# Kernel optimization log

Hardware: AMD Instinct MI355X
Metric: run time of the kernel (lower is better)

Reference implementation:

```python
import jax, jax.numpy as jnp
import numpy as np
from jax import lax

B, DIM, F, H, W = 2, 256, 4, 16, 16
HEADS, DIM_HEAD, GROUPS = 8, 64, 4
INNER = HEADS * DIM_HEAD            # 512
OFF_DIMS = INNER // GROUPS          # 128
CPB_DIM = DIM // 4                  # 64
DS = (2, 2, 2)                      # downsample_factor
OFFSET_SCALE = (2.0, 2.0, 2.0)


def norm_coords(coords, sizes):
    # coords: (..., 3) in (f, h, w) index units -> normalized to [-1, 1]
    s = jnp.array([max(sizes[0] - 1, 1), max(sizes[1] - 1, 1), max(sizes[2] - 1, 1)], dtype=coords.dtype)
    return 2.0 * coords / s - 1.0


def grid_sample_3d(vol, grid):
    # Faithful to F.grid_sample(..., mode='bilinear', padding_mode='zeros', align_corners=False)
    # vol: (N, C, D, H, W); grid: (N, P, 3) with last dim (x, y, z) -> (W, H, D) axes
    N, C, D, Hh, Ww = vol.shape
    P = grid.shape[1]
    ix = ((grid[..., 0] + 1.0) * Ww - 1.0) * 0.5
    iy = ((grid[..., 1] + 1.0) * Hh - 1.0) * 0.5
    iz = ((grid[..., 2] + 1.0) * D - 1.0) * 0.5
    x0, y0, z0 = jnp.floor(ix), jnp.floor(iy), jnp.floor(iz)
    tx, ty, tz = ix - x0, iy - y0, iz - z0
    vol_flat = vol.reshape(N, C, D * Hh * Ww)
    out = jnp.zeros((N, C, P), vol.dtype)
    for dz in (0, 1):
        for dy in (0, 1):
            for dx in (0, 1):
                xc, yc, zc = x0 + dx, y0 + dy, z0 + dz
                wgt = (jnp.where(dx, tx, 1.0 - tx) * jnp.where(dy, ty, 1.0 - ty) * jnp.where(dz, tz, 1.0 - tz))
                valid = ((xc >= 0) & (xc < Ww) & (yc >= 0) & (yc < Hh) & (zc >= 0) & (zc < D))
                xi = jnp.clip(xc, 0, Ww - 1).astype(jnp.int32)
                yi = jnp.clip(yc, 0, Hh - 1).astype(jnp.int32)
                zi = jnp.clip(zc, 0, D - 1).astype(jnp.int32)
                idx = (zi * Hh + yi) * Ww + xi                      # (N, P)
                vals = jnp.take_along_axis(vol_flat, jnp.broadcast_to(idx[:, None, :], (N, C, P)), axis=2)
                out = out + vals * (wgt * valid)[:, None, :]
    return out


def setup_inputs():
    key = jax.random.key(0)
    ks = jax.random.split(key, 16)
    r = lambda i, shape: jax.random.normal(ks[i], shape, dtype=jnp.float32) * 0.05
    return {
        'x': jax.random.normal(ks[0], (B, DIM, F, H, W), dtype=jnp.float32),
        'wq': r(1, (GROUPS, OFF_DIMS, DIM // GROUPS)),
        'wk': r(2, (GROUPS, OFF_DIMS, DIM // GROUPS)),
        'wv': r(3, (GROUPS, OFF_DIMS, DIM // GROUPS)),
        'off_dw_w': r(4, (OFF_DIMS, 1, 4, 4, 4)),
        'off_dw_b': r(5, (OFF_DIMS,)),
        'off_pw_w': r(6, (3, OFF_DIMS)),
        'cpb_w0': r(7, (3, CPB_DIM)),
        'cpb_b0': r(8, (CPB_DIM,)),
        'cpb_w1': r(9, (CPB_DIM, CPB_DIM)),
        'cpb_b1': r(10, (CPB_DIM,)),
        'cpb_w2': r(11, (CPB_DIM, HEADS // GROUPS)),
        'cpb_b2': r(12, (HEADS // GROUPS,)),
        'wo': r(13, (DIM, INNER)),
        'bo': r(14, (DIM,)),
    }


def reference(x, wq, wk, wv, off_dw_w, off_dw_b, off_pw_w, cpb_w0, cpb_b0, cpb_w1, cpb_b1, cpb_w2, cpb_b2, wo, bo):
    b = x.shape[0]
    f, h, w = x.shape[-3:]
    Pq = f * h * w
    scale = DIM_HEAD ** -0.5

    # grouped 1x1 conv to queries: channels are (g, d_out) ordered
    xg = x.reshape(b, GROUPS, DIM // GROUPS, Pq)
    q = jnp.einsum('bgip,goi->bgop', xg, wq)                        # (b, G, 128, Pq)

    # learned offsets: depthwise strided conv -> GELU -> 1x1 -> tanh -> scale
    gq = q.reshape(b * GROUPS, OFF_DIMS, f, h, w)
    off = lax.conv_general_dilated(gq, off_dw_w, window_strides=DS, padding=[(1, 1)] * 3,
                                   dimension_numbers=('NCDHW', 'OIDHW', 'NCDHW'),
                                   feature_group_count=OFF_DIMS)
    off = jax.nn.gelu(off + off_dw_b[None, :, None, None, None], approximate=False)
    off = jnp.einsum('ncdhw,oc->nodhw', off, off_pw_w)              # (bG, 3, fd, hd, wd)
    off = jnp.tanh(off) * jnp.array(OFFSET_SCALE, off.dtype)[None, :, None, None, None]

    fd, hd, wd = off.shape[-3:]
    Pj = fd * hd * wd
    base = jnp.stack(jnp.meshgrid(jnp.arange(fd), jnp.arange(hd), jnp.arange(wd), indexing='ij'), axis=0).astype(off.dtype)
    vgrid = base[None] + off
    vgrid_scaled = norm_coords(jnp.moveaxis(vgrid, 1, -1), (fd, hd, wd))  # (bG, fd, hd, wd, 3)
    grid_kv = vgrid_scaled.reshape(b * GROUPS, Pj, 3)

    # irregular gather of grouped features at deformed locations
    kv = grid_sample_3d(x.reshape(b * GROUPS, DIM // GROUPS, f, h, w), grid_kv)  # (bG, 64, Pj)
    kvg = kv.reshape(b, GROUPS, DIM // GROUPS, Pj)
    k = jnp.einsum('bgip,goi->bgop', kvg, wk)
    v = jnp.einsum('bgip,goi->bgop', kvg, wv)

    qh = (q * scale).reshape(b, HEADS, DIM_HEAD, Pq)
    kh = k.reshape(b, HEADS, DIM_HEAD, Pj)
    vh = v.reshape(b, HEADS, DIM_HEAD, Pj)
    sim = jnp.einsum('bhdi,bhdj->bhij', qh, kh)                     # (b, H, Pq, Pj)

    # CPB relative-position bias over (log-signed) pairwise grid differences
    baseq = jnp.stack(jnp.meshgrid(jnp.arange(f), jnp.arange(h), jnp.arange(w), indexing='ij'), axis=-1).astype(x.dtype)
    grid_q = norm_coords(baseq, (f, h, w)).reshape(Pq, 3)
    pos = grid_q[None, :, None, :] - grid_kv[:, None, :, :]         # (bG, Pq, Pj, 3)
    bias = jnp.sign(pos) * jnp.log1p(jnp.abs(pos))
    bias = jax.nn.relu(bias @ cpb_w0 + cpb_b0)
    bias = jax.nn.relu(bias @ cpb_w1 + cpb_b1)
    bias = bias @ cpb_w2 + cpb_b2                                   # (bG, Pq, Pj, H//G)
    bias = bias.reshape(b, GROUPS, Pq, Pj, HEADS // GROUPS)
    bias = jnp.transpose(bias, (0, 1, 4, 2, 3)).reshape(b, HEADS, Pq, Pj)

    attn = jax.nn.softmax(sim + bias, axis=-1)
    out = jnp.einsum('bhij,bhdj->bhdi', attn, vh).reshape(b, INNER, Pq)
    out = jnp.einsum('bcp,oc->bop', out, wo) + bo[None, :, None]
    return out.reshape(b, DIM, f, h, w)
```

## Files before the change

kernel.cpp:

```cpp
#include <hip/hip_runtime.h>
#include <hip/hip_bf16.h>
#include <hip/hip_fp16.h>
#include <math.h>

#define BB 2
#define DIMC 256
#define FF 4
#define HH 16
#define WW 16
#define GRP 4
#define CPG 64
#define ODIM 128
#define PQ 1024
#define PJ 128
#define NBG 8
#define INNERC 512

typedef _Float16 f16x8 __attribute__((ext_vector_type(8)));
typedef _Float16 f16x4 __attribute__((ext_vector_type(4)));
typedef _Float16 f16x2 __attribute__((ext_vector_type(2)));
typedef float f32x4 __attribute__((ext_vector_type(4)));
typedef float f32x2 __attribute__((ext_vector_type(2)));

__global__ __launch_bounds__(512) void k_qdw(
    const float* __restrict__ x, const float* __restrict__ wq,
    const float* __restrict__ dww, const float* __restrict__ dwb,
    const float* __restrict__ wo, _Float16* __restrict__ woH, _Float16* __restrict__ woL,
    float* __restrict__ q, float* __restrict__ act) {
    __shared__ float qs[1024 * 4];
    int og = blockIdx.x & 31, bg = blockIdx.x >> 5;
    int b = bg >> 2, g = bg & 3;
    int o0 = og * 4;
    int tid = threadIdx.x;

    {
        int i = blockIdx.x * 512 + tid;
        float v = wo[i];
        _Float16 hh = (_Float16)v;
        woH[i] = hh;
        woL[i] = (_Float16)(v - (float)hh);
    }

    const float* xp = x + (size_t)(b * DIMC + g * CPG) * PQ;
    const float* wp = wq + (size_t)(g * ODIM + o0) * CPG;

    float accq[2][4] = {};
    #pragma unroll 8
    for (int i = 0; i < CPG; ++i) {
        float wv[4];
        #pragma unroll
        for (int k = 0; k < 4; ++k) wv[k] = wp[k * CPG + i];
        #pragma unroll
        for (int pi = 0; pi < 2; ++pi) {
            float xv = xp[(size_t)i * PQ + tid + pi * 512];
            #pragma unroll
            for (int k = 0; k < 4; ++k) accq[pi][k] += xv * wv[k];
        }
    }
    #pragma unroll
    for (int pi = 0; pi < 2; ++pi) {
        int p = tid + pi * 512;
        *(float4*)&qs[p * 4] = make_float4(accq[pi][0], accq[pi][1], accq[pi][2], accq[pi][3]);
        #pragma unroll
        for (int k = 0; k < 4; ++k)
            q[(size_t)(bg * ODIM + o0 + k) * PQ + p] = accq[pi][k];
    }
    __syncthreads();

    {
        int cl = tid & 3, j = tid >> 2;
        int c = o0 + cl;
        int xo = j & 7, yo = (j >> 3) & 7, zo = j >> 6;
        const float* wd = dww + c * 64;
        float acc = dwb[c];
        #pragma unroll
        for (int kz = 0; kz < 4; ++kz) {
            int z = 2 * zo - 1 + kz;
            if (z < 0 || z >= FF) continue;
            #pragma unroll
            for (int ky = 0; ky < 4; ++ky) {
                int y = 2 * yo - 1 + ky;
                if (y < 0 || y >= HH) continue;
                #pragma unroll
                for (int kx = 0; kx < 4; ++kx) {
                    int xx = 2 * xo - 1 + kx;
                    if (xx < 0 || xx >= WW) continue;
                    acc += qs[((z * HH + y) * WW + xx) * 4 + cl] * wd[(kz * 4 + ky) * 4 + kx];
                }
            }
        }
        act[((size_t)bg * PJ + j) * ODIM + c] =
            0.5f * acc * (1.0f + erff(acc * 0.70710678118654752f));
    }
}

__global__ __launch_bounds__(256) void k_kvf(
    const float* __restrict__ act, const float* __restrict__ pw,
    const float* __restrict__ x, const float* __restrict__ wk,
    const float* __restrict__ wv, float* __restrict__ gkv,
    _Float16* __restrict__ khT, _Float16* __restrict__ vhT) {
    __shared__ float red2[2][6];
    __shared__ float crd[2][3];
    __shared__ float kvs[2][64];
    int blk = blockIdx.x;
    int jt = blk & 63, bg = blk >> 6;
    int b = bg >> 2, g = bg & 3;
    int tid = threadIdx.x;
    int half = tid >> 7;
    int t = tid & 127;
    int j = jt * 2 + half;
    int wv_ = t >> 6;

    float val = act[((size_t)bg * PJ + j) * ODIM + t];
    float s0 = val * pw[t];
    float s1 = val * pw[ODIM + t];
    float s2 = val * pw[2 * ODIM + t];
    #pragma unroll
    for (int off = 32; off; off >>= 1) {
        s0 += __shfl_xor(s0, off);
        s1 += __shfl_xor(s1, off);
        s2 += __shfl_xor(s2, off);
    }
    if ((t & 63) == 0) {
        red2[half][wv_ * 3] = s0; red2[half][wv_ * 3 + 1] = s1; red2[half][wv_ * 3 + 2] = s2;
    }
    __syncthreads();
    if (t == 0) {
        s0 = red2[half][0] + red2[half][3];
        s1 = red2[half][1] + red2[half][4];
        s2 = red2[half][2] + red2[half][5];
        float xo = (float)(j & 7), yo = (float)((j >> 3) & 7), zo = (float)(j >> 6);
        float vf = zo + 2.f * tanhf(s0);
        float vh = yo + 2.f * tanhf(s1);
        float vw = xo + 2.f * tanhf(s2);
        float c0 = 2.f * vf - 1.f;
        float c1 = 2.f * vh / 7.f - 1.f;
        float c2 = 2.f * vw / 7.f - 1.f;
        crd[half][0] = c0; crd[half][1] = c1; crd[half][2] = c2;
        gkv[(bg * PJ + j) * 3 + 0] = c0;
        gkv[(bg * PJ + j) * 3 + 1] = c1;
        gkv[(bg * PJ + j) * 3 + 2] = c2;
    }
    __syncthreads();

    if (t < 64) {
        float ix = ((crd[half][0] + 1.f) * WW - 1.f) * 0.5f;
        float iy = ((crd[half][1] + 1.f) * HH - 1.f) * 0.5f;
        float iz = ((crd[half][2] + 1.f) * FF - 1.f) * 0.5f;
        float x0f = floorf(ix), y0f = floorf(iy), z0f = floorf(iz);
        float tx = ix - x0f, ty = iy - y0f, tz = iz - z0f;
        int x0 = (int)x0f, y0 = (int)y0f, z0 = (int)z0f;
        const float* vol = x + (size_t)(b * DIMC + g * CPG + t) * PQ;
        float acc = 0.f;
        #pragma unroll
        for (int dz = 0; dz < 2; ++dz) {
            int zc = z0 + dz;
            if (zc < 0 || zc >= FF) continue;
            float wz = dz ? tz : 1.f - tz;
            #pragma unroll
            for (int dy = 0; dy < 2; ++dy) {
                int yc = y0 + dy;
                if (yc < 0 || yc >= HH) continue;
                float wy = dy ? ty : 1.f - ty;
                #pragma unroll
                for (int dx = 0; dx < 2; ++dx) {
                    int xc = x0 + dx;
                    if (xc < 0 || xc >= WW) continue;
                    float wgt = wz * wy * (dx ? tx : 1.f - tx);
                    acc += vol[(zc * HH + yc) * WW + xc] * wgt;
                }
            }
        }
        kvs[half][t] = acc;
    }
    __syncthreads();

    const float* wkp = wk + (size_t)(g * ODIM + t) * CPG;
    const float* wvp = wv + (size_t)(g * ODIM + t) * CPG;
    float ak = 0.f, av = 0.f;
    #pragma unroll
    for (int i = 0; i < 64; i += 4) {
        float4 kv4 = *(const float4*)&kvs[half][i];
        float4 wk4 = *(const float4*)&wkp[i];
        float4 wv4 = *(const float4*)&wvp[i];
        ak += kv4.x * wk4.x + kv4.y * wk4.y + kv4.z * wk4.z + kv4.w * wk4.w;
        av += kv4.x * wv4.x + kv4.y * wv4.y + kv4.z * wv4.z + kv4.w * wv4.w;
    }
    {
        _Float16 khi = (_Float16)ak;
        khT[((size_t)(bg * 128 + j) * 2 + 0) * 128 + t] = khi;
        khT[((size_t)(bg * 128 + j) * 2 + 1) * 128 + t] = (_Float16)(ak - (float)khi);
        _Float16 vhi = (_Float16)av;
        vhT[((size_t)(bg * 128 + t) * 2 + 0) * 128 + j] = vhi;
        vhT[((size_t)(bg * 128 + t) * 2 + 1) * 128 + j] = (_Float16)(av - (float)vhi);
    }
}

__global__ __launch_bounds__(256) void k_bias(
    const float* __restrict__ gkv,
    const float* __restrict__ w0, const float* __restrict__ b0,
    const float* __restrict__ w1, const float* __restrict__ b1,
    const float* __restrict__ w2, const float* __restrict__ b2,
    float* __restrict__ biasG) {
    __shared__ __align__(16) float tbuf[4 * 2176];
    int blk = blockIdx.x;
    int mh = blk & 1, it = (blk >> 1) & 63, bg = blk >> 7;
    int tid = threadIdx.x;
    int w = tid >> 6, lane = tid & 63, col = lane & 15, quad = lane >> 4;

    uint4 bfr[2][4];
    #pragma unroll
    for (int kc = 0; kc < 2; ++kc)
        #pragma unroll
        for (int nt = 0; nt < 4; ++nt) {
            int n = nt * 16 + col;
            int kbase = kc * 32 + quad * 8;
            unsigned int pk[4];
            #pragma unroll
            for (int p = 0; p < 4; ++p) {
                f16x2 hv = {(_Float16)w1[(kbase + 2 * p) * 64 + n],
                            (_Float16)w1[(kbase + 2 * p + 1) * 64 + n]};
                pk[p] = *(unsigned int*)&hv;
            }
            bfr[kc][nt] = make_uint4(pk[0], pk[1], pk[2], pk[3]);
        }

    f16x2 w0a[2][4], w0b[2][4], w0c[2][4], b0h[2][4];
    #pragma unroll
    for (int kc = 0; kc < 2; ++kc) {
        int d0 = kc * 32 + quad * 8;
        #pragma unroll
        for (int pr = 0; pr < 4; ++pr) {
            w0a[kc][pr] = (f16x2){(_Float16)w0[d0 + 2 * pr], (_Float16)w0[d0 + 2 * pr + 1]};
            w0b[kc][pr] = (f16x2){(_Float16)w0[64 + d0 + 2 * pr], (_Float16)w0[64 + d0 + 2 * pr + 1]};
            w0c[kc][pr] = (f16x2){(_Float16)w0[128 + d0 + 2 * pr], (_Float16)w0[128 + d0 + 2 * pr + 1]};
            b0h[kc][pr] = (f16x2){(_Float16)b0[d0 + 2 * pr], (_Float16)b0[d0 + 2 * pr + 1]};
        }
    }
    f16x2 zero2 = {(_Float16)0.f, (_Float16)0.f};

    float g0r[4], g1r[4], g2r[4];
    #pragma unroll
    for (int mt = 0; mt < 4; ++mt) {
        int jr = (mh * 4 + mt) * 16 + col;
        g0r[mt] = gkv[(bg * PJ + jr) * 3 + 0];
        g1r[mt] = gkv[(bg * PJ + jr) * 3 + 1];
        g2r[mt] = gkv[(bg * PJ + jr) * 3 + 2];
    }
    float b1v[4]; f32x2 w2v[4];
    #pragma unroll
    for (int nt = 0; nt < 4; ++nt) {
        int jj = nt * 16 + col;
        b1v[nt] = b1[jj];
        w2v[nt] = *(const f32x2*)&w2[jj * 2];
    }
    f32x2 bias_b2 = *(const f32x2*)b2;
    f32x2* mytb = (f32x2*)&tbuf[w * 2176];
    float* bb = biasG + (size_t)((bg * 64 + it) * 2) * 2048;

    #pragma unroll 1
    for (int ii = 0; ii < 4; ++ii) {
        int il = w * 4 + ii;
        int i = it * 16 + il;
        int wq_ = i & 15, hq = (i >> 4) & 15, fq = i >> 8;
        float cq0 = 2.f * fq / 3.f - 1.f;
        float cq1 = 2.f * hq / 15.f - 1.f;
        float cq2 = 2.f * wq_ / 15.f - 1.f;

        f16x2 t0h[4], t1h[4], t2h[4];
        #pragma unroll
        for (int mt = 0; mt < 4; ++mt) {
            float p0 = cq0 - g0r[mt];
            float p1 = cq1 - g1r[mt];
            float p2 = cq2 - g2r[mt];
            float t0 = copysignf(__logf(1.f + fabsf(p0)), p0);
            float t1 = copysignf(__logf(1.f + fabsf(p1)), p1);
            float t2 = copysignf(__logf(1.f + fabsf(p2)), p2);
            _Float16 h0 = (_Float16)t0, h1 = (_Float16)t1, h2 = (_Float16)t2;
            t0h[mt] = (f16x2){h0, h0};
            t1h[mt] = (f16x2){h1, h1};
            t2h[mt] = (f16x2){h2, h2};
        }
        f32x4 acc[4][4] = {};
        #pragma unroll
        for (int kc = 0; kc < 2; ++kc) {
            #pragma unroll
            for (int mt = 0; mt < 4; ++mt) {
                unsigned int pk[4];
                #pragma unroll
                for (int pr = 0; pr < 4; ++pr) {
                    f16x2 z = b0h[kc][pr];
                    z += t0h[mt] * w0a[kc][pr];
                    z += t1h[mt] * w0b[kc][pr];
                    z += t2h[mt] * w0c[kc][pr];
                    z = __builtin_elementwise_max(z, zero2);
                    pk[pr] = *(unsigned int*)&z;
                }
                uint4 afu = make_uint4(pk[0], pk[1], pk[2], pk[3]);
                f16x8 af = *(f16x8*)&afu;
                #pragma unroll
                for (int nt = 0; nt < 4; ++nt)
                    acc[mt][nt] = __builtin_amdgcn_mfma_f32_16x16x32_f16(
                        af, *(f16x8*)&bfr[kc][nt], acc[mt][nt], 0, 0, 0);
            }
        }
        #pragma unroll
        for (int mt = 0; mt < 4; ++mt)
            #pragma unroll
            for (int reg = 0; reg < 4; ++reg) {
                f32x2 pp = {0.f, 0.f};
                #pragma unroll
                for (int nt = 0; nt < 4; ++nt) {
                    float hv = fmaxf(acc[mt][nt][reg] + b1v[nt], 0.f);
                    pp += hv * w2v[nt];
                }
                mytb[(mt * 16 + quad * 4 + reg) * 17 + col] = pp;
            }
        f32x2 s = bias_b2;
        {
            const f32x2* pr2 = mytb + lane * 17;
            #pragma unroll
            for (int c = 0; c < 16; ++c) s += pr2[c];
        }
        int jl = mh * 64 + lane;
        bb[(size_t)il * 128 + jl] = s.x;
        bb[(size_t)(16 + il) * 128 + jl] = s.y;
    }
}

__global__ __launch_bounds__(256) void k_attn(
    const float* __restrict__ q, const _Float16* __restrict__ khT,
    const _Float16* __restrict__ vhT, const float* __restrict__ biasG,
    _Float16* __restrict__ outhH, _Float16* __restrict__ outhL) {
    __shared__ __align__(16) _Float16 attFh[2 * 16 * 136];
    __shared__ __align__(16) _Float16 attFl[2 * 16 * 136];
    __shared__ __align__(16) _Float16 qsFh[16 * 136];
    __shared__ __align__(16) _Float16 qsFl[16 * 136];
    __shared__ float smax[64];
    __shared__ float ssum[64];

    int blk = blockIdx.x;
    int it = blk & 63, bg = blk >> 6;
    int b = bg >> 2, g = bg & 3;
    int tid = threadIdx.x;
    int w = tid >> 6, lane = tid & 63, col = lane & 15, quad = lane >> 4;

    {
        int o = tid & 127, hf = tid >> 7;
        const float* qp = q + (size_t)(bg * ODIM + o) * PQ + it * 16 + hf * 8;
        float4 qa = *(const float4*)qp;
        float4 qb = *(const float4*)(qp + 4);
        float vals[8] = {qa.x, qa.y, qa.z, qa.w, qb.x, qb.y, qb.z, qb.w};
        #pragma unroll
        for (int k = 0; k < 8; ++k) {
            float v = vals[k] * 0.125f;
            _Float16 vhi = (_Float16)v;
            qsFh[(hf * 8 + k) * 136 + o] = vhi;
            qsFl[(hf * 8 + k) * 136 + o] = (_Float16)(v - (float)vhi);
        }
    }
    __syncthreads();

    int h = w >> 1, jh = w & 1;

    f16x8 aqh[2], aql[2];
    #pragma unroll
    for (int kc = 0; kc < 2; ++kc) {
        aqh[kc] = *(f16x8*)&qsFh[col * 136 + h * 64 + kc * 32 + quad * 8];
        aql[kc] = *(f16x8*)&qsFl[col * 136 + h * 64 + kc * 32 + quad * 8];
    }
    const float* bbase = biasG + (size_t)((bg * 64 + it) * 2 + h) * 2048;
    f32x4 acc[4];
    #pragma unroll
    for (int jt = 0; jt < 4; ++jt) {
        int j0 = jh * 64 + jt * 16;
        #pragma unroll
        for (int r = 0; r < 4; ++r)
            acc[jt][r] = bbase[(size_t)(quad * 4 + r) * 128 + j0 + col];
    }
    const _Float16* kbase = khT + (size_t)(bg * 128) * 256 + h * 64 + quad * 8;
    #pragma unroll
    for (int kc = 0; kc < 2; ++kc) {
        #pragma unroll
        for (int jt = 0; jt < 4; ++jt) {
            const _Float16* kp = kbase + (size_t)(jh * 64 + jt * 16 + col) * 256 + kc * 32;
            f16x8 bh = *(const f16x8*)kp;
            f16x8 bl = *(const f16x8*)(kp + 128);
            acc[jt] = __builtin_amdgcn_mfma_f32_16x16x32_f16(aqh[kc], bh, acc[jt], 0, 0, 0);
            acc[jt] = __builtin_amdgcn_mfma_f32_16x16x32_f16(aql[kc], bh, acc[jt], 0, 0, 0);
            acc[jt] = __builtin_amdgcn_mfma_f32_16x16x32_f16(aqh[kc], bl, acc[jt], 0, 0, 0);
        }
    }

    float mrow[4];
    #pragma unroll
    for (int r = 0; r < 4; ++r) {
        float m = fmaxf(fmaxf(acc[0][r], acc[1][r]), fmaxf(acc[2][r], acc[3][r]));
        #pragma unroll
        for (int off = 1; off <= 8; off <<= 1) m = fmaxf(m, __shfl_xor(m, off));
        mrow[r] = m;
    }
    if (col == 0) {
        #pragma unroll
        for (int r = 0; r < 4; ++r) smax[(h * 2 + jh) * 16 + quad * 4 + r] = mrow[r];
    }
    __syncthreads();
    #pragma unroll
    for (int r = 0; r < 4; ++r)
        mrow[r] = fmaxf(smax[(h * 2) * 16 + quad * 4 + r],
                        smax[(h * 2 + 1) * 16 + quad * 4 + r]);

    float lrow[4] = {0.f, 0.f, 0.f, 0.f};
    #pragma unroll
    for (int jt = 0; jt < 4; ++jt) {
        int j0 = jh * 64 + jt * 16;
        #pragma unroll
        for (int r = 0; r < 4; ++r) {
            float p = __expf(acc[jt][r] - mrow[r]);
            lrow[r] += p;
            _Float16 phi = (_Float16)p;
            attFh[(h * 16 + quad * 4 + r) * 136 + j0 + col] = phi;
            attFl[(h * 16 + quad * 4 + r) * 136 + j0 + col] = (_Float16)(p - (float)phi);
        }
    }
    #pragma unroll
    for (int r = 0; r < 4; ++r) {
        float l = lrow[r];
        #pragma unroll
        for (int off = 1; off <= 8; off <<= 1) l += __shfl_xor(l, off);
        lrow[r] = l;
    }
    if (col == 0) {
        #pragma unroll
        for (int r = 0; r < 4; ++r) ssum[(h * 2 + jh) * 16 + quad * 4 + r] = lrow[r];
    }
    __syncthreads();

    f16x8 pah[4], pal[4];
    #pragma unroll
    for (int kc = 0; kc < 4; ++kc) {
        pah[kc] = *(f16x8*)&attFh[(h * 16 + col) * 136 + kc * 32 + quad * 8];
        pal[kc] = *(f16x8*)&attFl[(h * 16 + col) * 136 + kc * 32 + quad * 8];
    }
    float rinv[4];
    #pragma unroll
    for (int r = 0; r < 4; ++r)
        rinv[r] = 1.f / (ssum[(h * 2) * 16 + quad * 4 + r] +
                         ssum[(h * 2 + 1) * 16 + quad * 4 + r]);

    f32x4 oacc[2] = {};
    int chl0 = jh * 32 + col;
    #pragma unroll
    for (int kc = 0; kc < 4; ++kc) {
        #pragma unroll
        for (int nt = 0; nt < 2; ++nt) {
            int chl = chl0 + nt * 16;
            const _Float16* vp = vhT + (size_t)(bg * 128 + h * 64 + chl) * 256 + kc * 32 + quad * 8;
            f16x8 vh8 = *(const f16x8*)vp;
            f16x8 vl8 = *(const f16x8*)(vp + 128);
            oacc[nt] = __builtin_amdgcn_mfma_f32_16x16x32_f16(pah[kc], vh8, oacc[nt], 0, 0, 0);
            oacc[nt] = __builtin_amdgcn_mfma_f32_16x16x32_f16(pal[kc], vh8, oacc[nt], 0, 0, 0);
            oacc[nt] = __builtin_amdgcn_mfma_f32_16x16x32_f16(pah[kc], vl8, oacc[nt], 0, 0, 0);
        }
    }
    #pragma unroll
    for (int nt = 0; nt < 2; ++nt) {
        int chl = chl0 + nt * 16;
        #pragma unroll
        for (int r = 0; r < 4; ++r) {
            float val = oacc[nt][r] * rinv[r];
            size_t idx = ((size_t)(b * PQ + it * 16 + quad * 4 + r)) * INNERC
                         + g * 128 + h * 64 + chl;
            _Float16 vhi = (_Float16)val;
            outhH[idx] = vhi;
            outhL[idx] = (_Float16)(val - (float)vhi);
        }
    }
}

__global__ __launch_bounds__(256) void k_out(
    const _Float16* __restrict__ outhH, const _Float16* __restrict__ outhL,
    const _Float16* __restrict__ woH, const _Float16* __restrict__ woL,
    const float* __restrict__ bo, float* __restrict__ out) {
    int blk = blockIdx.x;
    int ntb = blk & 7, mtb = blk >> 3;
    int tid = threadIdx.x;
    int w = tid >> 6, lane = tid & 63, col = lane & 15, quad = lane >> 4;
    int m0 = mtb * 64 + w * 16;
    int o0 = ntb * 32;

    const _Float16* ahb = outhH + (size_t)(m0 + col) * INNERC + quad * 8;
    const _Float16* alb = outhL + (size_t)(m0 + col) * INNERC + quad * 8;

    f32x4 oacc[2] = {};
    #pragma unroll 4
    for (int ks = 0; ks < 16; ++ks) {
        f16x8 ah = *(const f16x8*)(ahb + ks * 32);
        f16x8 al = *(const f16x8*)(alb + ks * 32);
        #pragma unroll
        for (int nt = 0; nt < 2; ++nt) {
            const _Float16* bp = woH + (size_t)(o0 + nt * 16 + col) * INNERC + ks * 32 + quad * 8;
            const _Float16* lp = woL + (size_t)(o0 + nt * 16 + col) * INNERC + ks * 32 + quad * 8;
            f16x8 bh = *(const f16x8*)bp;
            f16x8 bl = *(const f16x8*)lp;
            oacc[nt] = __builtin_amdgcn_mfma_f32_16x16x32_f16(ah, bh, oacc[nt], 0, 0, 0);
            oacc[nt] = __builtin_amdgcn_mfma_f32_16x16x32_f16(al, bh, oacc[nt], 0, 0, 0);
            oacc[nt] = __builtin_amdgcn_mfma_f32_16x16x32_f16(ah, bl, oacc[nt], 0, 0, 0);
        }
    }
    #pragma unroll
    for (int nt = 0; nt < 2; ++nt) {
        int o = o0 + nt * 16 + col;
        float bv = bo[o];
        int m = m0 + quad * 4;
        int bb = m >> 10, p = m & 1023;
        float4 st = make_float4(oacc[nt][0] + bv, oacc[nt][1] + bv,
                                oacc[nt][2] + bv, oacc[nt][3] + bv);
        *(float4*)&out[((size_t)(bb * DIMC + o)) * PQ + p] = st;
    }
}

extern "C" void kernel_launch(void* const* d_in, const int* in_sizes, int n_in,
                              void* d_out, int out_size, void* d_ws, size_t ws_size,
                              hipStream_t stream) {
    const float* x   = (const float*)d_in[0];
    const float* wq  = (const float*)d_in[1];
    const float* wk  = (const float*)d_in[2];
    const float* wv  = (const float*)d_in[3];
    const float* dww = (const float*)d_in[4];
    const float* dwb = (const float*)d_in[5];
    const float* pw  = (const float*)d_in[6];
    const float* w0  = (const float*)d_in[7];
    const float* b0  = (const float*)d_in[8];
    const float* w1  = (const float*)d_in[9];
    const float* b1  = (const float*)d_in[10];
    const float* w2  = (const float*)d_in[11];
    const float* b2  = (const float*)d_in[12];
    const float* wo  = (const float*)d_in[13];
    const float* bo  = (const float*)d_in[14];
    float* out = (float*)d_out;

    float* ws_f  = (float*)d_ws;
    float* q     = ws_f;
    float* act   = q + 1048576;
    float* gkv   = act + 131072;
    _Float16* khT   = (_Float16*)(gkv + 3072);
    _Float16* vhT   = khT + 262144;
    _Float16* outhH = vhT + 262144;
    _Float16* outhL = outhH + 1048576;
    _Float16* woH   = outhL + 1048576;
    _Float16* woL   = woH + 131072;
    float* biasG = (float*)(woL + 131072);

    k_qdw<<<256, 512, 0, stream>>>(x, wq, dww, dwb, wo, woH, woL, q, act);
    k_kvf<<<512, 256, 0, stream>>>(act, pw, x, wk, wv, gkv, khT, vhT);
    k_bias<<<1024, 256, 0, stream>>>(gkv, w0, b0, w1, b1, w2, b2, biasG);
    k_attn<<<512, 256, 0, stream>>>(q, khT, vhT, biasG, outhH, outhL);
    k_out<<<256, 256, 0, stream>>>(outhH, outhL, woH, woL, bo, out);
}
```

Baseline: 165.5 us.

## Fuse CPB bias MLP into attention kernel and hoist shared first-layer terms

Merges the bias-MLP kernel into the attention kernel, so each block computes its own 32x128 bias tile in shared memory. This removes the global biasG write and read-back and one launch. Within a block every query row shares f and h, so the first MLP layer's f/h contributions plus bias are precomputed once per key into LDS, leaving only the w term per row. The cost is more shared memory per block and a longer serial prologue before attention, which may lower occupancy.

```diff
diff --git a/kernel.cpp b/kernel.cpp
--- a/kernel.cpp
+++ b/kernel.cpp
@@ -196,17 +196,50 @@
     }
 }
 
-__global__ __launch_bounds__(256) void k_bias(
-    const float* __restrict__ gkv,
+__global__ __launch_bounds__(256) void k_cpa(
+    const float* __restrict__ q, const _Float16* __restrict__ khT,
+    const _Float16* __restrict__ vhT, const float* __restrict__ gkv,
     const float* __restrict__ w0, const float* __restrict__ b0,
     const float* __restrict__ w1, const float* __restrict__ b1,
     const float* __restrict__ w2, const float* __restrict__ b2,
-    float* __restrict__ biasG) {
+    _Float16* __restrict__ outhH, _Float16* __restrict__ outhL) {
     __shared__ __align__(16) float tbuf[4 * 2176];
+    __shared__ __align__(16) float biasL[2 * 16 * 132];
+    __shared__ __align__(16) _Float16 baseL[128 * 72];
+    __shared__ float smax[64];
+    __shared__ float ssum[64];
+
     int blk = blockIdx.x;
-    int mh = blk & 1, it = (blk >> 1) & 63, bg = blk >> 7;
+    int it = blk & 63, bg = blk >> 6;
+    int b = bg >> 2, g = bg & 3;
     int tid = threadIdx.x;
     int w = tid >> 6, lane = tid & 63, col = lane & 15, quad = lane >> 4;
+
+    float cq0c = 2.f * (float)(it >> 4) / 3.f - 1.f;
+    float cq1c = 2.f * (float)(it & 15) / 15.f - 1.f;
+
+    {
+        int j0_ = tid & 127, dh_ = tid >> 7;
+        float g0 = gkv[(bg * PJ + j0_) * 3 + 0];
+        float g1 = gkv[(bg * PJ + j0_) * 3 + 1];
+        float p0 = cq0c - g0, p1 = cq1c - g1;
+        float t0 = copysignf(__logf(1.f + fabsf(p0)), p0);
+        float t1 = copysignf(__logf(1.f + fabsf(p1)), p1);
+        int d0_ = dh_ * 32;
+        #pragma unroll
+        for (int dd = 0; dd < 32; dd += 4) {
+            int d = d0_ + dd;
+            float4 wa = *(const float4*)&w0[d];
+            float4 wb = *(const float4*)&w0[64 + d];
+            float4 bb4 = *(const float4*)&b0[d];
+            f16x4 pk4;
+            pk4[0] = (_Float16)(t0 * wa.x + t1 * wb.x + bb4.x);
+            pk4[1] = (_Float16)(t0 * wa.y + t1 * wb.y + bb4.y);
+            pk4[2] = (_Float16)(t0 * wa.z + t1 * wb.z + bb4.z);
+            pk4[3] = (_Float16)(t0 * wa.w + t1 * wb.w + bb4.w);
+            *(f16x4*)&baseL[j0_ * 72 + d] = pk4;
+        }
+    }
 
     uint4 bfr[2][4];
     #pragma unroll
@@ -225,28 +258,22 @@
             bfr[kc][nt] = make_uint4(pk[0], pk[1], pk[2], pk[3]);
         }
 
-    f16x2 w0a[2][4], w0b[2][4], w0c[2][4], b0h[2][4];
+    f16x2 w0c[2][4];
     #pragma unroll
     for (int kc = 0; kc < 2; ++kc) {
         int d0 = kc * 32 + quad * 8;
         #pragma unroll
-        for (int pr = 0; pr < 4; ++pr) {
-            w0a[kc][pr] = (f16x2){(_Float16)w0[d0 + 2 * pr], (_Float16)w0[d0 + 2 * pr + 1]};
-            w0b[kc][pr] = (f16x2){(_Float16)w0[64 + d0 + 2 * pr], (_Float16)w0[64 + d0 + 2 * pr + 1]};
-            w0c[kc][pr] = (f16x2){(_Float16)w0[128 + d0 + 2 * pr], (_Float16)w0[128 + d0 + 2 * pr + 1]};
-            b0h[kc][pr] = (f16x2){(_Float16)b0[d0 + 2 * pr], (_Float16)b0[d0 + 2 * pr + 1]};
-        }
+        for (int pr = 0; pr < 4; ++pr)
+            w0c[kc][pr] = (f16x2){(_Float16)w0[128 + d0 + 2 * pr],
+                                  (_Float16)w0[128 + d0 + 2 * pr + 1]};
     }
     f16x2 zero2 = {(_Float16)0.f, (_Float16)0.f};
 
-    float g0r[4], g1r[4], g2r[4];
-    #pragma unroll
-    for (int mt = 0; mt < 4; ++mt) {
-        int jr = (mh * 4 + mt) * 16 + col;
-        g0r[mt] = gkv[(bg * PJ + jr) * 3 + 0];
-        g1r[mt] = gkv[(bg * PJ + jr) * 3 + 1];
-        g2r[mt] = gkv[(bg * PJ + jr) * 3 + 2];
-    }
+    float g2r[8];
+    #pragma unroll
+    for (int mtg = 0; mtg < 8; ++mtg)
+        g2r[mtg] = gkv[(bg * PJ + mtg * 16 + col) * 3 + 2];
+
     float b1v[4]; f32x2 w2v[4];
     #pragma unroll
     for (int nt = 0; nt < 4; ++nt) {
@@ -256,94 +283,76 @@
     }
     f32x2 bias_b2 = *(const f32x2*)b2;
     f32x2* mytb = (f32x2*)&tbuf[w * 2176];
-    float* bb = biasG + (size_t)((bg * 64 + it) * 2) * 2048;
+
+    __syncthreads();
 
     #pragma unroll 1
     for (int ii = 0; ii < 4; ++ii) {
         int il = w * 4 + ii;
-        int i = it * 16 + il;
-        int wq_ = i & 15, hq = (i >> 4) & 15, fq = i >> 8;
-        float cq0 = 2.f * fq / 3.f - 1.f;
-        float cq1 = 2.f * hq / 15.f - 1.f;
-        float cq2 = 2.f * wq_ / 15.f - 1.f;
-
-        f16x2 t0h[4], t1h[4], t2h[4];
-        #pragma unroll
-        for (int mt = 0; mt < 4; ++mt) {
-            float p0 = cq0 - g0r[mt];
-            float p1 = cq1 - g1r[mt];
-            float p2 = cq2 - g2r[mt];
-            float t0 = copysignf(__logf(1.f + fabsf(p0)), p0);
-            float t1 = copysignf(__logf(1.f + fabsf(p1)), p1);
-            float t2 = copysignf(__logf(1.f + fabsf(p2)), p2);
-            _Float16 h0 = (_Float16)t0, h1 = (_Float16)t1, h2 = (_Float16)t2;
-            t0h[mt] = (f16x2){h0, h0};
-            t1h[mt] = (f16x2){h1, h1};
-            t2h[mt] = (f16x2){h2, h2};
-        }
-        f32x4 acc[4][4] = {};
-        #pragma unroll
-        for (int kc = 0; kc < 2; ++kc) {
+        float cq2 = 2.f * (float)il / 15.f - 1.f;
+
+        #pragma unroll 1
+        for (int mh = 0; mh < 2; ++mh) {
+            f16x2 t2h[4];
             #pragma unroll
             for (int mt = 0; mt < 4; ++mt) {
-                unsigned int pk[4];
+                float p2 = cq2 - g2r[mh * 4 + mt];
+                float t2 = copysignf(__logf(1.f + fabsf(p2)), p2);
+                _Float16 h2 = (_Float16)t2;
+                t2h[mt] = (f16x2){h2, h2};
+            }
+            f32x4 acc[4][4] = {};
+            #pragma unroll
+            for (int kc = 0; kc < 2; ++kc) {
                 #pragma unroll
-                for (int pr = 0; pr < 4; ++pr) {
-                    f16x2 z = b0h[kc][pr];
-                    z += t0h[mt] * w0a[kc][pr];
-                    z += t1h[mt] * w0b[kc][pr];
-                    z += t2h[mt] * w0c[kc][pr];
-                    z = __builtin_elementwise_max(z, zero2);
-                    pk[pr] = *(unsigned int*)&z;
+                for (int mt = 0; mt < 4; ++mt) {
+                    int jr = (mh * 4 + mt) * 16 + col;
+                    f16x8 bse = *(const f16x8*)&baseL[jr * 72 + kc * 32 + quad * 8];
+                    unsigned int pk[4];
+                    #pragma unroll
+                    for (int pr = 0; pr < 4; ++pr) {
+                        f16x2 z = (f16x2){bse[2 * pr], bse[2 * pr + 1]}
+                                  + t2h[mt] * w0c[kc][pr];
+                        z = __builtin_elementwise_max(z, zero2);
+                        pk[pr] = *(unsigned int*)&z;
+                    }
+                    uint4 afu = make_uint4(pk[0], pk[1], pk[2], pk[3]);
+                    f16x8 af = *(f16x8*)&afu;
+                    #pragma unroll
+                    for (int nt = 0; nt < 4; ++nt)
+                        acc[mt][nt] = __builtin_amdgcn_mfma_f32_16x16x32_f16(
+                            af, *(f16x8*)&bfr[kc][nt], acc[mt][nt], 0, 0, 0);
                 }
-                uint4 afu = make_uint4(pk[0], pk[1], pk[2], pk[3]);
-                f16x8 af = *(f16x8*)&afu;
+            }
+            #pragma unroll
+            for (int mt = 0; mt < 4; ++mt)
                 #pragma unroll
-                for (int nt = 0; nt < 4; ++nt)
-                    acc[mt][nt] = __builtin_amdgcn_mfma_f32_16x16x32_f16(
-                        af, *(f16x8*)&bfr[kc][nt], acc[mt][nt], 0, 0, 0);
+                for (int reg = 0; reg < 4; ++reg) {
+                    f32x2 pp = {0.f, 0.f};
+                    #pragma unroll
+                    for (int nt = 0; nt < 4; ++nt) {
+                        float hv = fmaxf(acc[mt][nt][reg] + b1v[nt], 0.f);
+                        pp += hv * w2v[nt];
+                    }
+                    mytb[(mt * 16 + quad * 4 + reg) * 17 + col] = pp;
+                }
+            f32x2 s = bias_b2;
+            {
+                const f32x2* pr2 = mytb + lane * 17;
+                #pragma unroll
+                for (int c = 0; c < 16; ++c) s += pr2[c];
             }
-        }
-        #pragma unroll
-        for (int mt = 0; mt < 4; ++mt)
-            #pragma unroll
-            for (int reg = 0; reg < 4; ++reg) {
-                f32x2 pp = {0.f, 0.f};
-                #pragma unroll
-                for (int nt = 0; nt < 4; ++nt) {
-                    float hv = fmaxf(acc[mt][nt][reg] + b1v[nt], 0.f);
-                    pp += hv * w2v[nt];
-                }
-                mytb[(mt * 16 + quad * 4 + reg) * 17 + col] = pp;
-            }
-        f32x2 s = bias_b2;
-        {
-            const f32x2* pr2 = mytb + lane * 17;
-            #pragma unroll
-            for (int c = 0; c < 16; ++c) s += pr2[c];
-        }
-        int jl = mh * 64 + lane;
-        bb[(size_t)il * 128 + jl] = s.x;
-        bb[(size_t)(16 + il) * 128 + jl] = s.y;
-    }
-}
-
-__global__ __launch_bounds__(256) void k_attn(
-    const float* __restrict__ q, const _Float16* __restrict__ khT,
-    const _Float16* __restrict__ vhT, const float* __restrict__ biasG,
-    _Float16* __restrict__ outhH, _Float16* __restrict__ outhL) {
-    __shared__ __align__(16) _Float16 attFh[2 * 16 * 136];
-    __shared__ __align__(16) _Float16 attFl[2 * 16 * 136];
-    __shared__ __align__(16) _Float16 qsFh[16 * 136];
-    __shared__ __align__(16) _Float16 qsFl[16 * 136];
-    __shared__ float smax[64];
-    __shared__ float ssum[64];
-
-    int blk = blockIdx.x;
-    int it = blk & 63, bg = blk >> 6;
-    int b = bg >> 2, g = bg & 3;
-    int tid = threadIdx.x;
-    int w = tid >> 6, lane = tid & 63, col = lane & 15, quad = lane >> 4;
+            int jl = mh * 64 + lane;
+            biasL[il * 132 + jl] = s.x;
+            biasL[(16 + il) * 132 + jl] = s.y;
+        }
+    }
+    __syncthreads();
+
+    _Float16* attFh = (_Float16*)tbuf;
+    _Float16* attFl = attFh + 4352;
+    _Float16* qsFh  = attFh + 8704;
+    _Float16* qsFl  = attFh + 10880;
 
     {
         int o = tid & 127, hf = tid >> 7;
@@ -369,14 +378,13 @@
         aqh[kc] = *(f16x8*)&qsFh[col * 136 + h * 64 + kc * 32 + quad * 8];
         aql[kc] = *(f16x8*)&qsFl[col * 136 + h * 64 + kc * 32 + quad * 8];
     }
-    const float* bbase = biasG + (size_t)((bg * 64 + it) * 2 + h) * 2048;
     f32x4 acc[4];
     #pragma unroll
     for (int jt = 0; jt < 4; ++jt) {
         int j0 = jh * 64 + jt * 16;
         #pragma unroll
         for (int r = 0; r < 4; ++r)
-            acc[jt][r] = bbase[(size_t)(quad * 4 + r) * 128 + j0 + col];
+            acc[jt][r] = biasL[(h * 16 + quad * 4 + r) * 132 + j0 + col];
     }
     const _Float16* kbase = khT + (size_t)(bg * 128) * 256 + h * 64 + quad * 8;
     #pragma unroll
@@ -550,11 +558,9 @@
     _Float16* outhL = outhH + 1048576;
     _Float16* woH   = outhL + 1048576;
     _Float16* woL   = woH + 131072;
-    float* biasG = (float*)(woL + 131072);
 
     k_qdw<<<256, 512, 0, stream>>>(x, wq, dww, dwb, wo, woH, woL, q, act);
     k_kvf<<<512, 256, 0, stream>>>(act, pw, x, wk, wv, gkv, khT, vhT);
-    k_bias<<<1024, 256, 0, stream>>>(gkv, w0, b0, w1, b1, w2, b2, biasG);
-    k_attn<<<512, 256, 0, stream>>>(q, khT, vhT, biasG, outhH, outhL);
+    k_cpa<<<512, 256, 0, stream>>>(q, khT, vhT, gkv, w0, b0, w1, b1, w2, b2, outhH, outhL);
     k_out<<<256, 256, 0, stream>>>(outhH, outhL, woH, woL, bo, out);
 }
```

New measurement: 148.1 us, median of 2. 1.12x faster.
